# Kernel tuning notes

Measured on AMD Instinct MI355X. Metric: run time of the kernel, lower is better.

Reference implementation:

```python
import jax, jax.numpy as jnp
import numpy as np

B, T, C = 2, 4096, 512
H, DH = 8, 64            # num_heads, num_head_channels (per-head dim after reshape)
COND = 512
SCALE = (DH // H) ** -0.5  # faithful to original: (num_head_channels // num_heads)**-0.5


def setup_inputs() -> dict:
    key = jax.random.key(0)
    ks = jax.random.split(key, 6)
    x = jax.random.normal(ks[0], (B, T, C), dtype=jnp.float32)
    condition = jax.random.normal(ks[1], (B, T, COND), dtype=jnp.float32)
    W_qk = jax.random.normal(ks[2], (COND, 2 * H * DH), dtype=jnp.float32) * (COND ** -0.5)
    W_v = jax.random.normal(ks[3], (C, H * DH), dtype=jnp.float32) * (C ** -0.5)
    W_u = jax.random.normal(ks[4], (H * DH, C), dtype=jnp.float32) * ((H * DH) ** -0.5)
    b_u = jax.random.normal(ks[5], (C,), dtype=jnp.float32) * 0.01
    return {"x": x, "condition": condition, "W_qk": W_qk, "W_v": W_v, "W_u": W_u, "b_u": b_u}


def reference(x, condition, W_qk, W_v, W_u, b_u):
    b, t, _ = x.shape
    qk = condition @ W_qk                                  # [b, t, 2*H*DH]
    q, k = jnp.split(qk, 2, axis=-1)
    q = q.reshape(b, t, H, DH).transpose(0, 2, 1, 3)       # [b, H, t, DH]
    k = k.reshape(b, t, H, DH).transpose(0, 2, 1, 3)
    v = (x @ W_v).reshape(b, t, H, DH).transpose(0, 2, 1, 3)
    q = q * SCALE
    dots = jnp.einsum('bhid,bhjd->bhij', q, k)             # [b, H, t, t] (1 GB score matrix)
    attn = jax.nn.softmax(dots, axis=-1)
    out = jnp.einsum('bhij,bhjd->bhid', attn, v)           # [b, H, t, DH]
    out = out.transpose(0, 2, 1, 3).reshape(b, t, H * DH)
    return out @ W_u + b_u
```

## Files before the change

### kernel.cpp

```cpp
#include <hip/hip_runtime.h>

#define B_SZ 2
#define T_SZ 4096

typedef unsigned short u16;
typedef __attribute__((ext_vector_type(8))) short short8;
typedef __attribute__((ext_vector_type(4))) float f32x4;
typedef __attribute__((ext_vector_type(4))) unsigned short u16x4;

#define CEXP 0.51006973f

__device__ __forceinline__ u16 f2bf(float f) {
    unsigned int u;
    __builtin_memcpy(&u, &f, 4);
    u = (u + 0x7fffu + ((u >> 16) & 1u)) >> 16;
    return (u16)u;
}
__device__ __forceinline__ unsigned int rbits(float f) {
    unsigned int u;
    __builtin_memcpy(&u, &f, 4);
    return u + 0x8000u;
}
__device__ __forceinline__ f32x4 mfma16(short8 a, short8 b, f32x4 c) {
    return __builtin_amdgcn_mfma_f32_16x16x32_bf16(a, b, c, 0, 0, 0);
}

__global__ void k_prep(const float* __restrict__ Wqk, const float* __restrict__ Wv,
                       const float* __restrict__ Wu, u16* __restrict__ Wqk_t,
                       u16* __restrict__ Wv_t, u16* __restrict__ Wu_t) {
    int blk = blockIdx.x, tid = threadIdx.x;
    __shared__ u16 T[64][72];
    const float* src; u16* dst; int N, ti;
    if (blk < 128)      { src = Wqk; dst = Wqk_t; N = 1024; ti = blk; }
    else if (blk < 192) { src = Wv;  dst = Wv_t;  N = 512;  ti = blk - 128; }
    else                { src = Wu;  dst = Wu_t;  N = 512;  ti = blk - 192; }
    int nt = N >> 6;
    int bi = ti / nt, bj = ti - bi * nt;
    int kb = bi * 64, nb = bj * 64;
    int r = tid >> 2, c4 = (tid & 3) * 16;
#pragma unroll
    for (int jj = 0; jj < 4; ++jj) {
        float4 v = *(const float4*)(src + (size_t)(kb + r) * N + nb + c4 + jj * 4);
        u16x4 w = { f2bf(v.x), f2bf(v.y), f2bf(v.z), f2bf(v.w) };
        *(u16x4*)(&T[r][c4 + jj * 4]) = w;
    }
    __syncthreads();
#pragma unroll
    for (int jj = 0; jj < 4; ++jj) {
        int c = c4 + jj * 4;
        u16x4 w = { T[c][r], T[c + 1][r], T[c + 2][r], T[c + 3][r] };
        *(u16x4*)(dst + (size_t)(nb + r) * 512 + kb + c) = w;
    }
}

template <typename OutT, int MODE, bool AF32, bool BF32, int TM, int TN>
__device__ __forceinline__ void gemm_body(int m0, int n0,
                                          const void* __restrict__ Ap, const void* __restrict__ Bp,
                                          const float* __restrict__ bias, OutT* __restrict__ C,
                                          OutT* __restrict__ C2, u16* As, u16* Bs) {
    const int K = 512;
    constexpr int BK = 64;
    constexpr int MI = TM / 32, NJ = TN / 32;
    constexpr int NAF = TM / 16, NAB = TM / 32;
    constexpr int NBF = TN / 16, NBB = TN / 32;
    int tid = threadIdx.x;
    int wave = tid >> 6, lane = tid & 63, l16 = lane & 15, q = lane >> 4;
    int mo = (wave & 1) * (TM / 2), no = (wave >> 1) * (TN / 2);

    f32x4 acc[MI][NJ];
#pragma unroll
    for (int i = 0; i < MI; ++i)
#pragma unroll
        for (int j = 0; j < NJ; ++j) acc[i][j] = (f32x4){0.f, 0.f, 0.f, 0.f};

    const float* Af = (const float*)Ap; const u16* Ab = (const u16*)Ap;
    const float* Bf = (const float*)Bp; const u16* Bb = (const u16*)Bp;

    const float* apf[NAF > 0 ? NAF : 1]; const u16* apb[NAB > 0 ? NAB : 1];
    const float* bpf[NBF > 0 ? NBF : 1]; const u16* bpb[NBB > 0 ? NBB : 1];
    float4 raf[NAF > 0 ? NAF : 1], rbf[NBF > 0 ? NBF : 1];
    short8 rab[NAB > 0 ? NAB : 1], rbb[NBB > 0 ? NBB : 1];

    if constexpr (AF32) {
#pragma unroll
        for (int jj = 0; jj < NAF; ++jj) {
            int id = tid + 256 * jj;
            apf[jj] = Af + (size_t)(m0 + (id >> 4)) * K + (id & 15) * 4;
            raf[jj] = *(const float4*)(apf[jj]);
        }
    } else {
#pragma unroll
        for (int jj = 0; jj < NAB; ++jj) {
            int id = tid + 256 * jj;
            apb[jj] = Ab + (size_t)(m0 + (id >> 3)) * K + (id & 7) * 8;
            rab[jj] = *(const short8*)(apb[jj]);
        }
    }
    if constexpr (BF32) {
#pragma unroll
        for (int jj = 0; jj < NBF; ++jj) {
            int id = tid + 256 * jj;
            bpf[jj] = Bf + (size_t)(n0 + (id >> 4)) * K + (id & 15) * 4;
            rbf[jj] = *(const float4*)(bpf[jj]);
        }
    } else {
#pragma unroll
        for (int jj = 0; jj < NBB; ++jj) {
            int id = tid + 256 * jj;
            bpb[jj] = Bb + (size_t)(n0 + (id >> 3)) * K + (id & 7) * 8;
            rbb[jj] = *(const short8*)(bpb[jj]);
        }
    }

#pragma unroll 1
    for (int k0 = 0; k0 < K; k0 += BK) {
        __syncthreads();
        if constexpr (AF32) {
#pragma unroll
            for (int jj = 0; jj < NAF; ++jj) {
                int id = tid + 256 * jj;
                u16x4 w = { f2bf(raf[jj].x), f2bf(raf[jj].y), f2bf(raf[jj].z), f2bf(raf[jj].w) };
                *(u16x4*)(&As[(id >> 4) * 72 + (id & 15) * 4]) = w;
            }
        } else {
#pragma unroll
            for (int jj = 0; jj < NAB; ++jj) {
                int id = tid + 256 * jj;
                *(short8*)(&As[(id >> 3) * 72 + (id & 7) * 8]) = rab[jj];
            }
        }
        if constexpr (BF32) {
#pragma unroll
            for (int jj = 0; jj < NBF; ++jj) {
                int id = tid + 256 * jj;
                u16x4 w = { f2bf(rbf[jj].x), f2bf(rbf[jj].y), f2bf(rbf[jj].z), f2bf(rbf[jj].w) };
                *(u16x4*)(&Bs[(id >> 4) * 72 + (id & 15) * 4]) = w;
            }
        } else {
#pragma unroll
            for (int jj = 0; jj < NBB; ++jj) {
                int id = tid + 256 * jj;
                *(short8*)(&Bs[(id >> 3) * 72 + (id & 7) * 8]) = rbb[jj];
            }
        }
        __syncthreads();

        int kadv = (k0 + BK < K) ? BK : 0;
        if constexpr (AF32) {
#pragma unroll
            for (int jj = 0; jj < NAF; ++jj) { apf[jj] += kadv; raf[jj] = *(const float4*)(apf[jj]); }
        } else {
#pragma unroll
            for (int jj = 0; jj < NAB; ++jj) { apb[jj] += kadv; rab[jj] = *(const short8*)(apb[jj]); }
        }
        if constexpr (BF32) {
#pragma unroll
            for (int jj = 0; jj < NBF; ++jj) { bpf[jj] += kadv; rbf[jj] = *(const float4*)(bpf[jj]); }
        } else {
#pragma unroll
            for (int jj = 0; jj < NBB; ++jj) { bpb[jj] += kadv; rbb[jj] = *(const short8*)(bpb[jj]); }
        }
        __builtin_amdgcn_sched_barrier(0);

#pragma unroll
        for (int kk = 0; kk < 2; ++kk) {
            short8 af[MI], bf[NJ];
#pragma unroll
            for (int i = 0; i < MI; ++i)
                af[i] = *(const short8*)(&As[(mo + i * 16 + l16) * 72 + kk * 32 + q * 8]);
#pragma unroll
            for (int j = 0; j < NJ; ++j)
                bf[j] = *(const short8*)(&Bs[(no + j * 16 + l16) * 72 + kk * 32 + q * 8]);
#pragma unroll
            for (int i = 0; i < MI; ++i)
#pragma unroll
                for (int j = 0; j < NJ; ++j) acc[i][j] = mfma16(af[i], bf[j], acc[i][j]);
        }
    }

#pragma unroll
    for (int i = 0; i < MI; ++i) {
        int mb = m0 + mo + i * 16 + q * 4;
#pragma unroll
        for (int j = 0; j < NJ; ++j) {
            int nc = n0 + no + j * 16 + l16;
            if constexpr (MODE == 0) {
                float4 bb = *(const float4*)(bias + mb);
                float4 w = { acc[i][j][0] + bb.x, acc[i][j][1] + bb.y,
                             acc[i][j][2] + bb.z, acc[i][j][3] + bb.w };
                *(float4*)(&C[(size_t)nc * 512 + mb]) = w;
            } else if constexpr (MODE == 1) {
                int b = nc >> 12, t = nc & 4095;
                int h = (mb & 511) >> 6, d = mb & 63;
                size_t addr = ((size_t)((b * 8 + h) * 4096 + t)) * 64 + d;
                if (mb < 512) {
                    u16x4 w = { f2bf(acc[i][j][0] * CEXP), f2bf(acc[i][j][1] * CEXP),
                                f2bf(acc[i][j][2] * CEXP), f2bf(acc[i][j][3] * CEXP) };
                    *(u16x4*)(&C[addr]) = w;
                } else {
                    u16x4 w = { f2bf(acc[i][j][0]), f2bf(acc[i][j][1]),
                                f2bf(acc[i][j][2]), f2bf(acc[i][j][3]) };
                    *(u16x4*)(&C2[addr]) = w;
                }
            } else {
                int b = mb >> 12, t = mb & 4095;
                int kt = t >> 6, k64 = t & 63;
                int h = nc >> 6, d = nc & 63;
                size_t addr = ((((size_t)(b * 8 + h) * 64 + kt) * 64 + d) << 6) + k64;
                u16x4 w = { f2bf(acc[i][j][0]), f2bf(acc[i][j][1]),
                            f2bf(acc[i][j][2]), f2bf(acc[i][j][3]) };
                *(u16x4*)(&C[addr]) = w;
            }
        }
    }
}

__global__ __launch_bounds__(256) void k_qkv(const u16* __restrict__ Wqk_t, const float* __restrict__ cond,
                                             const float* __restrict__ x, const u16* __restrict__ Wv_t,
                                             u16* __restrict__ Qh, u16* __restrict__ Kh,
                                             u16* __restrict__ Vb) {
    __shared__ __align__(16) u16 smem[(128 + 128) * 72];
    u16* As = smem;
    u16* Bs = smem + 128 * 72;
    int bid = blockIdx.x;
    if (bid < 512) {
        int bx = bid >> 6, by = bid & 63;
        gemm_body<u16, 1, false, true, 128, 128>(bx * 128, by * 128, Wqk_t, cond, nullptr, Qh, Kh, As, Bs);
    } else {
        int bid2 = bid - 512;
        int by = bid2 >> 6, bx = bid2 & 63;
        gemm_body<u16, 2, true, false, 128, 128>(bx * 128, by * 128, x, Wv_t, nullptr, Vb, nullptr, As, Bs);
    }
}

__global__ __launch_bounds__(256) void k_out(const u16* __restrict__ Wu_t, const u16* __restrict__ at,
                                             const float* __restrict__ bu, float* __restrict__ out) {
    __shared__ __align__(16) u16 smem[(128 + 128) * 72];
    int bid = blockIdx.x;
    int bx = bid >> 6, by = bid & 63;
    gemm_body<float, 0, false, false, 128, 128>(bx * 128, by * 128, Wu_t, at, bu, out, nullptr,
                                                smem, smem + 128 * 72);
}

__global__ __launch_bounds__(512) void k_flash(const u16* __restrict__ Qh, const u16* __restrict__ Kh,
                                               const u16* __restrict__ Vb, u16* __restrict__ o) {
    int bid = blockIdx.x;
    int h = bid & 7, qt = (bid >> 3) & 31, b = bid >> 8;
    int tid = threadIdx.x;
    int wave = tid >> 6, lane = tid & 63, l16 = lane & 15, q = lane >> 4;
    int ks = wave >> 2, w4 = wave & 3;
    int t256 = tid & 255;

    __shared__ __align__(16) u16 smem[19456];
    u16* Kt = smem + ks * 8704;
    u16* Vt = Kt + 64 * 64;

    int head = b * 8 + h;
    short8 qf[2][2];
#pragma unroll
    for (int g = 0; g < 2; ++g) {
        const u16* qp = Qh + ((size_t)head * 4096 + qt * 128 + g * 64 + w4 * 16 + l16) * 64 + q * 8;
        qf[g][0] = *(const short8*)(qp);
        qf[g][1] = *(const short8*)(qp + 32);
    }

    const u16* kb = Kh + (size_t)head * 4096 * 64;
    const u16* vb = Vb + (size_t)head * 4096 * 64;

    int r0 = t256 >> 3, g0 = t256 & 7;
    int sr = (r0 & 3) | (((r0 >> 3) & 1) << 2);
    u16* kw0 = &Kt[r0 * 64 + ((g0 ^ sr) << 3)];
    u16* kw1 = kw0 + 32 * 64;
    u16* vw0 = &Vt[r0 * 72 + g0 * 8];
    u16* vw1 = vw0 + 32 * 72;

    f32x4 oacc[2][4];
#pragma unroll
    for (int g = 0; g < 2; ++g)
#pragma unroll
        for (int c = 0; c < 4; ++c) oacc[g][c] = (f32x4){0.f, 0.f, 0.f, 0.f};
    f32x4 lacc[2];
    lacc[0] = (f32x4){0.f, 0.f, 0.f, 0.f};
    lacc[1] = (f32x4){0.f, 0.f, 0.f, 0.f};
    const short8 ones = { 0x3F80, 0x3F80, 0x3F80, 0x3F80, 0x3F80, 0x3F80, 0x3F80, 0x3F80 };
    int pi0 = (l16 >> 2) * 8 + (l16 & 3);
    int sq = l16 & 7;

    size_t off0 = (size_t)(ks * 32 + (qt & 31)) * 4096;
    short8 rk0 = *(const short8*)(kb + off0 + t256 * 8);
    short8 rk1 = *(const short8*)(kb + off0 + t256 * 8 + 2048);
    short8 rv0 = *(const short8*)(vb + off0 + t256 * 8);
    short8 rv1 = *(const short8*)(vb + off0 + t256 * 8 + 2048);

#pragma unroll 1
    for (int it = 0; it < 32; ++it) {
        __syncthreads();
        *(short8*)kw0 = rk0;
        *(short8*)kw1 = rk1;
        *(short8*)vw0 = rv0;
        *(short8*)vw1 = rv1;
        __syncthreads();

        size_t offn = (size_t)(ks * 32 + ((qt + it + 1) & 31)) * 4096;
        rk0 = *(const short8*)(kb + offn + t256 * 8);
        rk1 = *(const short8*)(kb + offn + t256 * 8 + 2048);
        rv0 = *(const short8*)(vb + offn + t256 * 8);
        rv1 = *(const short8*)(vb + offn + t256 * 8 + 2048);
        __builtin_amdgcn_sched_barrier(0);

        __builtin_amdgcn_s_setprio(1);
#pragma unroll
        for (int kk = 0; kk < 2; ++kk) {
            const u16* ka = &Kt[(kk * 32 + pi0) * 64];
            short8 A00 = *(const short8*)(ka + ((q ^ sq) << 3));
            short8 A01 = *(const short8*)(ka + (((4 | q) ^ sq) << 3));
            short8 A10 = *(const short8*)(ka + 4 * 64 + ((q ^ sq) << 3));
            short8 A11 = *(const short8*)(ka + 4 * 64 + (((4 | q) ^ sq) << 3));
            short8 vfc[4];
#pragma unroll
            for (int c = 0; c < 4; ++c)
                vfc[c] = *(const short8*)(&Vt[(c * 16 + l16) * 72 + kk * 32 + q * 8]);

#pragma unroll
            for (int g = 0; g < 2; ++g) {
                f32x4 s0 = (f32x4){0.f, 0.f, 0.f, 0.f};
                f32x4 s1 = (f32x4){0.f, 0.f, 0.f, 0.f};
                s0 = mfma16(A00, qf[g][0], s0); s0 = mfma16(A01, qf[g][1], s0);
                s1 = mfma16(A10, qf[g][0], s1); s1 = mfma16(A11, qf[g][1], s1);

                uint4 pd;
                pd.x = __builtin_amdgcn_perm(rbits(__builtin_amdgcn_exp2f(s0[1])),
                                             rbits(__builtin_amdgcn_exp2f(s0[0])), 0x07060302u);
                pd.y = __builtin_amdgcn_perm(rbits(__builtin_amdgcn_exp2f(s0[3])),
                                             rbits(__builtin_amdgcn_exp2f(s0[2])), 0x07060302u);
                pd.z = __builtin_amdgcn_perm(rbits(__builtin_amdgcn_exp2f(s1[1])),
                                             rbits(__builtin_amdgcn_exp2f(s1[0])), 0x07060302u);
                pd.w = __builtin_amdgcn_perm(rbits(__builtin_amdgcn_exp2f(s1[3])),
                                             rbits(__builtin_amdgcn_exp2f(s1[2])), 0x07060302u);
                short8 pf;
                __builtin_memcpy(&pf, &pd, 16);

                lacc[g] = mfma16(ones, pf, lacc[g]);
#pragma unroll
                for (int c = 0; c < 4; ++c)
                    oacc[g][c] = mfma16(vfc[c], pf, oacc[g][c]);
            }
        }
        __builtin_amdgcn_s_setprio(0);
    }

    __syncthreads();
    float* red = (float*)smem;
    if (ks == 1) {
        float* rp = red + ((w4 * 64 + lane) * 37);
#pragma unroll
        for (int g = 0; g < 2; ++g)
#pragma unroll
            for (int c = 0; c < 4; ++c)
#pragma unroll
                for (int r = 0; r < 4; ++r) rp[g * 16 + c * 4 + r] = oacc[g][c][r];
        rp[32] = lacc[0][0];
        rp[33] = lacc[1][0];
    }
    __syncthreads();
    if (ks == 0) {
        const float* rp = red + ((w4 * 64 + lane) * 37);
#pragma unroll
        for (int g = 0; g < 2; ++g) {
#pragma unroll
            for (int c = 0; c < 4; ++c)
#pragma unroll
                for (int r = 0; r < 4; ++r) oacc[g][c][r] += rp[g * 16 + c * 4 + r];
            float inv = 1.f / (lacc[g][0] + rp[32 + g]);
            u16* ob = o + (size_t)(b * T_SZ + qt * 128 + g * 64 + w4 * 16 + l16) * 512 + h * 64 + q * 4;
#pragma unroll
            for (int c = 0; c < 4; ++c) {
                u16x4 w = { f2bf(oacc[g][c][0] * inv), f2bf(oacc[g][c][1] * inv),
                            f2bf(oacc[g][c][2] * inv), f2bf(oacc[g][c][3] * inv) };
                *(u16x4*)(ob + c * 16) = w;
            }
        }
    }
}

extern "C" void kernel_launch(void* const* d_in, const int* in_sizes, int n_in,
                              void* d_out, int out_size, void* d_ws, size_t ws_size,
                              hipStream_t stream) {
    const float* x    = (const float*)d_in[0];
    const float* cond = (const float*)d_in[1];
    const float* Wqk  = (const float*)d_in[2];
    const float* Wv   = (const float*)d_in[3];
    const float* Wu   = (const float*)d_in[4];
    const float* bu   = (const float*)d_in[5];
    float* out = (float*)d_out;

    const size_t MT = (size_t)B_SZ * T_SZ;
    u16* qh_ws = (u16*)d_ws;
    u16* kh_ws = qh_ws + MT * 512;
    u16* vb_ws = kh_ws + MT * 512;
    u16* at_ws = vb_ws + MT * 512;
    u16* Wqk_t = at_ws + MT * 512;
    u16* Wv_t  = Wqk_t + (size_t)1024 * 512;
    u16* Wu_t  = Wv_t + (size_t)512 * 512;

    k_prep<<<256, 256, 0, stream>>>(Wqk, Wv, Wu, Wqk_t, Wv_t, Wu_t);
    k_qkv<<<768, 256, 0, stream>>>(Wqk_t, cond, x, Wv_t, qh_ws, kh_ws, vb_ws);
    k_flash<<<512, 512, 0, stream>>>(qh_ws, kh_ws, vb_ws, at_ws);
    k_out<<<256, 256, 0, stream>>>(Wu_t, at_ws, bu, out);
}
```

Before: 207.7 us.

## Fuse all four stages into one persistent kernel with grid barriers

Replaces the four separate launches (weight prep, QKV GEMM, flash attention, output GEMM) with a single 512-block kernel that runs each stage in turn, separated by atomic-counter grid barriers. The GEMMs now use 512-thread blocks with 128x256 tiles, and the register prefetch of the next K slice is dropped, so loads for a slice are issued right before it is used. This removes launch gaps and inter-kernel tail effects. In exchange, many blocks sit idle in the GEMM stages, all blocks must spin at each barrier, and the design depends on all 512 blocks being co-resident to avoid deadlock.

```diff
diff --git a/kernel.cpp b/kernel.cpp
--- a/kernel.cpp
+++ b/kernel.cpp
@@ -25,164 +25,129 @@
     return __builtin_amdgcn_mfma_f32_16x16x32_bf16(a, b, c, 0, 0, 0);
 }
 
-__global__ void k_prep(const float* __restrict__ Wqk, const float* __restrict__ Wv,
-                       const float* __restrict__ Wu, u16* __restrict__ Wqk_t,
-                       u16* __restrict__ Wv_t, u16* __restrict__ Wu_t) {
-    int blk = blockIdx.x, tid = threadIdx.x;
-    __shared__ u16 T[64][72];
-    const float* src; u16* dst; int N, ti;
-    if (blk < 128)      { src = Wqk; dst = Wqk_t; N = 1024; ti = blk; }
-    else if (blk < 192) { src = Wv;  dst = Wv_t;  N = 512;  ti = blk - 128; }
-    else                { src = Wu;  dst = Wu_t;  N = 512;  ti = blk - 192; }
-    int nt = N >> 6;
-    int bi = ti / nt, bj = ti - bi * nt;
-    int kb = bi * 64, nb = bj * 64;
-    int r = tid >> 2, c4 = (tid & 3) * 16;
-#pragma unroll
-    for (int jj = 0; jj < 4; ++jj) {
-        float4 v = *(const float4*)(src + (size_t)(kb + r) * N + nb + c4 + jj * 4);
-        u16x4 w = { f2bf(v.x), f2bf(v.y), f2bf(v.z), f2bf(v.w) };
-        *(u16x4*)(&T[r][c4 + jj * 4]) = w;
-    }
+struct GBar { unsigned int cnt; unsigned int p0[15]; unsigned int gen; unsigned int p1[15]; };
+__device__ GBar g_bar[3];
+#define NBLK 512
+
+__device__ __forceinline__ void gridbar(int i) {
     __syncthreads();
-#pragma unroll
-    for (int jj = 0; jj < 4; ++jj) {
-        int c = c4 + jj * 4;
-        u16x4 w = { T[c][r], T[c + 1][r], T[c + 2][r], T[c + 3][r] };
-        *(u16x4*)(dst + (size_t)(nb + r) * 512 + kb + c) = w;
-    }
-}
-
-template <typename OutT, int MODE, bool AF32, bool BF32, int TM, int TN>
-__device__ __forceinline__ void gemm_body(int m0, int n0,
-                                          const void* __restrict__ Ap, const void* __restrict__ Bp,
-                                          const float* __restrict__ bias, OutT* __restrict__ C,
-                                          OutT* __restrict__ C2, u16* As, u16* Bs) {
+    if (threadIdx.x == 0) {
+        unsigned int g = __hip_atomic_load(&g_bar[i].gen, __ATOMIC_ACQUIRE, __HIP_MEMORY_SCOPE_AGENT);
+        unsigned int a = __hip_atomic_fetch_add(&g_bar[i].cnt, 1u, __ATOMIC_ACQ_REL, __HIP_MEMORY_SCOPE_AGENT);
+        if (a == NBLK - 1u) {
+            __hip_atomic_store(&g_bar[i].cnt, 0u, __ATOMIC_RELAXED, __HIP_MEMORY_SCOPE_AGENT);
+            __hip_atomic_fetch_add(&g_bar[i].gen, 1u, __ATOMIC_RELEASE, __HIP_MEMORY_SCOPE_AGENT);
+        } else {
+            while (__hip_atomic_load(&g_bar[i].gen, __ATOMIC_ACQUIRE, __HIP_MEMORY_SCOPE_AGENT) == g)
+                __builtin_amdgcn_s_sleep(2);
+        }
+    }
+    __syncthreads();
+}
+
+template <typename OutT, int MODE, bool AF32, bool BF32>
+__device__ void gemm512(int m0, int n0, const void* __restrict__ Ap, const void* __restrict__ Bp,
+                        const float* __restrict__ bias, OutT* __restrict__ C,
+                        OutT* __restrict__ C2, u16* smem) {
     const int K = 512;
-    constexpr int BK = 64;
-    constexpr int MI = TM / 32, NJ = TN / 32;
-    constexpr int NAF = TM / 16, NAB = TM / 32;
-    constexpr int NBF = TN / 16, NBB = TN / 32;
+    u16* As = smem;
+    u16* Bs = smem + 128 * 72;
     int tid = threadIdx.x;
     int wave = tid >> 6, lane = tid & 63, l16 = lane & 15, q = lane >> 4;
-    int mo = (wave & 1) * (TM / 2), no = (wave >> 1) * (TN / 2);
-
-    f32x4 acc[MI][NJ];
-#pragma unroll
-    for (int i = 0; i < MI; ++i)
-#pragma unroll
-        for (int j = 0; j < NJ; ++j) acc[i][j] = (f32x4){0.f, 0.f, 0.f, 0.f};
+    int mo = (wave & 1) * 64, no = (wave >> 1) * 64;
+
+    f32x4 acc[4][4];
+#pragma unroll
+    for (int i = 0; i < 4; ++i)
+#pragma unroll
+        for (int j = 0; j < 4; ++j) acc[i][j] = (f32x4){0.f, 0.f, 0.f, 0.f};
 
     const float* Af = (const float*)Ap; const u16* Ab = (const u16*)Ap;
     const float* Bf = (const float*)Bp; const u16* Bb = (const u16*)Bp;
 
-    const float* apf[NAF > 0 ? NAF : 1]; const u16* apb[NAB > 0 ? NAB : 1];
-    const float* bpf[NBF > 0 ? NBF : 1]; const u16* bpb[NBB > 0 ? NBB : 1];
-    float4 raf[NAF > 0 ? NAF : 1], rbf[NBF > 0 ? NBF : 1];
-    short8 rab[NAB > 0 ? NAB : 1], rbb[NBB > 0 ? NBB : 1];
-
-    if constexpr (AF32) {
-#pragma unroll
-        for (int jj = 0; jj < NAF; ++jj) {
-            int id = tid + 256 * jj;
-            apf[jj] = Af + (size_t)(m0 + (id >> 4)) * K + (id & 15) * 4;
-            raf[jj] = *(const float4*)(apf[jj]);
-        }
-    } else {
-#pragma unroll
-        for (int jj = 0; jj < NAB; ++jj) {
-            int id = tid + 256 * jj;
-            apb[jj] = Ab + (size_t)(m0 + (id >> 3)) * K + (id & 7) * 8;
-            rab[jj] = *(const short8*)(apb[jj]);
-        }
-    }
-    if constexpr (BF32) {
-#pragma unroll
-        for (int jj = 0; jj < NBF; ++jj) {
-            int id = tid + 256 * jj;
-            bpf[jj] = Bf + (size_t)(n0 + (id >> 4)) * K + (id & 15) * 4;
-            rbf[jj] = *(const float4*)(bpf[jj]);
-        }
-    } else {
-#pragma unroll
-        for (int jj = 0; jj < NBB; ++jj) {
-            int id = tid + 256 * jj;
-            bpb[jj] = Bb + (size_t)(n0 + (id >> 3)) * K + (id & 7) * 8;
-            rbb[jj] = *(const short8*)(bpb[jj]);
-        }
-    }
-
 #pragma unroll 1
-    for (int k0 = 0; k0 < K; k0 += BK) {
+    for (int k0 = 0; k0 < K; k0 += 64) {
+        float4 raf[AF32 ? 4 : 1]; short8 rab[AF32 ? 1 : 2];
+        float4 rbf[BF32 ? 8 : 1]; short8 rbb[BF32 ? 1 : 4];
+        if constexpr (AF32) {
+#pragma unroll
+            for (int jj = 0; jj < 4; ++jj) {
+                int id = tid + 512 * jj;
+                raf[jj] = *(const float4*)(Af + (size_t)(m0 + (id >> 4)) * K + k0 + (id & 15) * 4);
+            }
+        } else {
+#pragma unroll
+            for (int jj = 0; jj < 2; ++jj) {
+                int id = tid + 512 * jj;
+                rab[jj] = *(const short8*)(Ab + (size_t)(m0 + (id >> 3)) * K + k0 + (id & 7) * 8);
+            }
+        }
+        if constexpr (BF32) {
+#pragma unroll
+            for (int jj = 0; jj < 8; ++jj) {
+                int id = tid + 512 * jj;
+                rbf[jj] = *(const float4*)(Bf + (size_t)(n0 + (id >> 4)) * K + k0 + (id & 15) * 4);
+            }
+        } else {
+#pragma unroll
+            for (int jj = 0; jj < 4; ++jj) {
+                int id = tid + 512 * jj;
+                rbb[jj] = *(const short8*)(Bb + (size_t)(n0 + (id >> 3)) * K + k0 + (id & 7) * 8);
+            }
+        }
+        __builtin_amdgcn_sched_barrier(0);
         __syncthreads();
         if constexpr (AF32) {
 #pragma unroll
-            for (int jj = 0; jj < NAF; ++jj) {
-                int id = tid + 256 * jj;
+            for (int jj = 0; jj < 4; ++jj) {
+                int id = tid + 512 * jj;
                 u16x4 w = { f2bf(raf[jj].x), f2bf(raf[jj].y), f2bf(raf[jj].z), f2bf(raf[jj].w) };
                 *(u16x4*)(&As[(id >> 4) * 72 + (id & 15) * 4]) = w;
             }
         } else {
 #pragma unroll
-            for (int jj = 0; jj < NAB; ++jj) {
-                int id = tid + 256 * jj;
+            for (int jj = 0; jj < 2; ++jj) {
+                int id = tid + 512 * jj;
                 *(short8*)(&As[(id >> 3) * 72 + (id & 7) * 8]) = rab[jj];
             }
         }
         if constexpr (BF32) {
 #pragma unroll
-            for (int jj = 0; jj < NBF; ++jj) {
-                int id = tid + 256 * jj;
+            for (int jj = 0; jj < 8; ++jj) {
+                int id = tid + 512 * jj;
                 u16x4 w = { f2bf(rbf[jj].x), f2bf(rbf[jj].y), f2bf(rbf[jj].z), f2bf(rbf[jj].w) };
                 *(u16x4*)(&Bs[(id >> 4) * 72 + (id & 15) * 4]) = w;
             }
         } else {
 #pragma unroll
-            for (int jj = 0; jj < NBB; ++jj) {
-                int id = tid + 256 * jj;
+            for (int jj = 0; jj < 4; ++jj) {
+                int id = tid + 512 * jj;
                 *(short8*)(&Bs[(id >> 3) * 72 + (id & 7) * 8]) = rbb[jj];
             }
         }
         __syncthreads();
 
-        int kadv = (k0 + BK < K) ? BK : 0;
-        if constexpr (AF32) {
-#pragma unroll
-            for (int jj = 0; jj < NAF; ++jj) { apf[jj] += kadv; raf[jj] = *(const float4*)(apf[jj]); }
-        } else {
-#pragma unroll
-            for (int jj = 0; jj < NAB; ++jj) { apb[jj] += kadv; rab[jj] = *(const short8*)(apb[jj]); }
-        }
-        if constexpr (BF32) {
-#pragma unroll
-            for (int jj = 0; jj < NBF; ++jj) { bpf[jj] += kadv; rbf[jj] = *(const float4*)(bpf[jj]); }
-        } else {
-#pragma unroll
-            for (int jj = 0; jj < NBB; ++jj) { bpb[jj] += kadv; rbb[jj] = *(const short8*)(bpb[jj]); }
-        }
-        __builtin_amdgcn_sched_barrier(0);
-
 #pragma unroll
         for (int kk = 0; kk < 2; ++kk) {
-            short8 af[MI], bf[NJ];
-#pragma unroll
-            for (int i = 0; i < MI; ++i)
+            short8 af[4], bf[4];
+#pragma unroll
+            for (int i = 0; i < 4; ++i)
                 af[i] = *(const short8*)(&As[(mo + i * 16 + l16) * 72 + kk * 32 + q * 8]);
 #pragma unroll
-            for (int j = 0; j < NJ; ++j)
+            for (int j = 0; j < 4; ++j)
                 bf[j] = *(const short8*)(&Bs[(no + j * 16 + l16) * 72 + kk * 32 + q * 8]);
 #pragma unroll
-            for (int i = 0; i < MI; ++i)
-#pragma unroll
-                for (int j = 0; j < NJ; ++j) acc[i][j] = mfma16(af[i], bf[j], acc[i][j]);
-        }
-    }
-
-#pragma unroll
-    for (int i = 0; i < MI; ++i) {
+            for (int i = 0; i < 4; ++i)
+#pragma unroll
+                for (int j = 0; j < 4; ++j) acc[i][j] = mfma16(af[i], bf[j], acc[i][j]);
+        }
+    }
+
+#pragma unroll
+    for (int i = 0; i < 4; ++i) {
         int mb = m0 + mo + i * 16 + q * 4;
 #pragma unroll
-        for (int j = 0; j < NJ; ++j) {
+        for (int j = 0; j < 4; ++j) {
             int nc = n0 + no + j * 16 + l16;
             if constexpr (MODE == 0) {
                 float4 bb = *(const float4*)(bias + mb);
@@ -215,44 +180,15 @@
     }
 }
 
-__global__ __launch_bounds__(256) void k_qkv(const u16* __restrict__ Wqk_t, const float* __restrict__ cond,
-                                             const float* __restrict__ x, const u16* __restrict__ Wv_t,
-                                             u16* __restrict__ Qh, u16* __restrict__ Kh,
-                                             u16* __restrict__ Vb) {
-    __shared__ __align__(16) u16 smem[(128 + 128) * 72];
-    u16* As = smem;
-    u16* Bs = smem + 128 * 72;
-    int bid = blockIdx.x;
-    if (bid < 512) {
-        int bx = bid >> 6, by = bid & 63;
-        gemm_body<u16, 1, false, true, 128, 128>(bx * 128, by * 128, Wqk_t, cond, nullptr, Qh, Kh, As, Bs);
-    } else {
-        int bid2 = bid - 512;
-        int by = bid2 >> 6, bx = bid2 & 63;
-        gemm_body<u16, 2, true, false, 128, 128>(bx * 128, by * 128, x, Wv_t, nullptr, Vb, nullptr, As, Bs);
-    }
-}
-
-__global__ __launch_bounds__(256) void k_out(const u16* __restrict__ Wu_t, const u16* __restrict__ at,
-                                             const float* __restrict__ bu, float* __restrict__ out) {
-    __shared__ __align__(16) u16 smem[(128 + 128) * 72];
-    int bid = blockIdx.x;
-    int bx = bid >> 6, by = bid & 63;
-    gemm_body<float, 0, false, false, 128, 128>(bx * 128, by * 128, Wu_t, at, bu, out, nullptr,
-                                                smem, smem + 128 * 72);
-}
-
-__global__ __launch_bounds__(512) void k_flash(const u16* __restrict__ Qh, const u16* __restrict__ Kh,
-                                               const u16* __restrict__ Vb, u16* __restrict__ o) {
-    int bid = blockIdx.x;
+__device__ void flash_dev(int bid, const u16* __restrict__ Qh, const u16* __restrict__ Kh,
+                          const u16* __restrict__ Vb, u16* __restrict__ o, u16* sm) {
     int h = bid & 7, qt = (bid >> 3) & 31, b = bid >> 8;
     int tid = threadIdx.x;
     int wave = tid >> 6, lane = tid & 63, l16 = lane & 15, q = lane >> 4;
     int ks = wave >> 2, w4 = wave & 3;
     int t256 = tid & 255;
 
-    __shared__ __align__(16) u16 smem[19456];
-    u16* Kt = smem + ks * 8704;
+    u16* Kt = sm + ks * 8704;
     u16* Vt = Kt + 64 * 64;
 
     int head = b * 8 + h;
@@ -350,7 +286,7 @@
     }
 
     __syncthreads();
-    float* red = (float*)smem;
+    float* red = (float*)sm;
     if (ks == 1) {
         float* rp = red + ((w4 * 64 + lane) * 37);
 #pragma unroll
@@ -380,6 +316,62 @@
                 *(u16x4*)(ob + c * 16) = w;
             }
         }
+    }
+}
+
+__global__ __launch_bounds__(512, 4) void k_fused(
+    const float* __restrict__ x, const float* __restrict__ cond,
+    const float* __restrict__ Wqk, const float* __restrict__ Wv,
+    const float* __restrict__ Wu, const float* __restrict__ bu, float* __restrict__ out,
+    u16* __restrict__ Qh, u16* __restrict__ Kh, u16* __restrict__ Vb, u16* __restrict__ at,
+    u16* __restrict__ Wqk_t, u16* __restrict__ Wv_t, u16* __restrict__ Wu_t) {
+    __shared__ __align__(16) u16 smem[27648];
+    int bid = blockIdx.x, tid = threadIdx.x;
+
+    if (bid < 128) {
+        int half = tid >> 8, t256 = tid & 255;
+        int ti = bid * 2 + half;
+        u16 (*T)[72] = (u16(*)[72])(smem + half * 4608);
+        const float* src; u16* dst; int N, tt;
+        if (ti < 128)      { src = Wqk; dst = Wqk_t; N = 1024; tt = ti; }
+        else if (ti < 192) { src = Wv;  dst = Wv_t;  N = 512;  tt = ti - 128; }
+        else               { src = Wu;  dst = Wu_t;  N = 512;  tt = ti - 192; }
+        int nt = N >> 6;
+        int bi = tt / nt, bj = tt - bi * nt;
+        int kb = bi * 64, nb = bj * 64;
+        int r = t256 >> 2, c4 = (t256 & 3) * 16;
+#pragma unroll
+        for (int jj = 0; jj < 4; ++jj) {
+            float4 v = *(const float4*)(src + (size_t)(kb + r) * N + nb + c4 + jj * 4);
+            u16x4 w = { f2bf(v.x), f2bf(v.y), f2bf(v.z), f2bf(v.w) };
+            *(u16x4*)(&T[r][c4 + jj * 4]) = w;
+        }
+        __syncthreads();
+#pragma unroll
+        for (int jj = 0; jj < 4; ++jj) {
+            int c = c4 + jj * 4;
+            u16x4 w = { T[c][r], T[c + 1][r], T[c + 2][r], T[c + 3][r] };
+            *(u16x4*)(dst + (size_t)(nb + r) * 512 + kb + c) = w;
+        }
+    }
+    gridbar(0);
+
+    if (bid < 256) {
+        int bx = bid >> 5, by = bid & 31;
+        gemm512<u16, 1, false, true>(bx * 128, by * 256, Wqk_t, cond, nullptr, Qh, Kh, smem);
+    } else if (bid < 384) {
+        int id2 = bid - 256;
+        int m = id2 & 63, n = id2 >> 6;
+        gemm512<u16, 2, true, false>(m * 128, n * 256, x, Wv_t, nullptr, Vb, nullptr, smem);
+    }
+    gridbar(1);
+
+    flash_dev(bid, Qh, Kh, Vb, at, smem);
+    gridbar(2);
+
+    if (bid < 128) {
+        int bx = bid >> 5, by = bid & 31;
+        gemm512<float, 0, false, false>(bx * 128, by * 256, Wu_t, at, bu, out, nullptr, smem);
     }
 }
 
@@ -403,8 +395,6 @@
     u16* Wv_t  = Wqk_t + (size_t)1024 * 512;
     u16* Wu_t  = Wv_t + (size_t)512 * 512;
 
-    k_prep<<<256, 256, 0, stream>>>(Wqk, Wv, Wu, Wqk_t, Wv_t, Wu_t);
-    k_qkv<<<768, 256, 0, stream>>>(Wqk_t, cond, x, Wv_t, qh_ws, kh_ws, vb_ws);
-    k_flash<<<512, 512, 0, stream>>>(qh_ws, kh_ws, vb_ws, at_ws);
-    k_out<<<256, 256, 0, stream>>>(Wu_t, at_ws, bu, out);
-}
+    k_fused<<<512, 512, 0, stream>>>(x, cond, Wqk, Wv, Wu, bu, out,
+                                     qh_ws, kh_ws, vb_ws, at_ws, Wqk_t, Wv_t, Wu_t);
+}
```

Result: slower. 539.3 us (+159.6%).

## Double the flash-attention KV tile per iteration and swizzle the V LDS layout

Applied to the files above, without the earlier changes.

Each K/V-split group now stages 128 keys per iteration instead of 64, halving the loop trip count and the number of block-wide barriers. V is stored with an XOR swizzle in two 64-wide halves instead of padded rows. Register prefetch doubles to four short8 loads each for K and V per thread, and LDS use grows to 64 KB. This raises register pressure and may lower occupancy.

```diff
diff --git a/kernel.cpp b/kernel.cpp
--- a/kernel.cpp
+++ b/kernel.cpp
@@ -251,9 +251,9 @@
     int ks = wave >> 2, w4 = wave & 3;
     int t256 = tid & 255;
 
-    __shared__ __align__(16) u16 smem[19456];
-    u16* Kt = smem + ks * 8704;
-    u16* Vt = Kt + 64 * 64;
+    __shared__ __align__(16) u16 smem[32768];
+    u16* Kt = smem + ks * 16384;
+    u16* Vt = Kt + 8192;
 
     int head = b * 8 + h;
     short8 qf[2][2];
@@ -269,10 +269,12 @@
 
     int r0 = t256 >> 3, g0 = t256 & 7;
     int sr = (r0 & 3) | (((r0 >> 3) & 1) << 2);
-    u16* kw0 = &Kt[r0 * 64 + ((g0 ^ sr) << 3)];
-    u16* kw1 = kw0 + 32 * 64;
-    u16* vw0 = &Vt[r0 * 72 + g0 * 8];
-    u16* vw1 = vw0 + 32 * 72;
+    u16* kw[4]; u16* vw[4];
+#pragma unroll
+    for (int j = 0; j < 4; ++j) {
+        kw[j] = &Kt[(r0 + 32 * j) * 64 + ((g0 ^ sr) << 3)];
+        vw[j] = &Vt[(j >> 1) * 4096 + (r0 + 32 * (j & 1)) * 64 + ((g0 ^ sr) << 3)];
+    }
 
     f32x4 oacc[2][4];
 #pragma unroll
@@ -285,41 +287,46 @@
     const short8 ones = { 0x3F80, 0x3F80, 0x3F80, 0x3F80, 0x3F80, 0x3F80, 0x3F80, 0x3F80 };
     int pi0 = (l16 >> 2) * 8 + (l16 & 3);
     int sq = l16 & 7;
-
-    size_t off0 = (size_t)(ks * 32 + (qt & 31)) * 4096;
-    short8 rk0 = *(const short8*)(kb + off0 + t256 * 8);
-    short8 rk1 = *(const short8*)(kb + off0 + t256 * 8 + 2048);
-    short8 rv0 = *(const short8*)(vb + off0 + t256 * 8);
-    short8 rv1 = *(const short8*)(vb + off0 + t256 * 8 + 2048);
+    int sv = (l16 & 3) | (((l16 >> 3) & 1) << 2);
+    int st = qt & 15;
+
+    short8 rk[4], rv[4];
+    size_t off0 = (size_t)(ks * 16 + st) * 8192;
+#pragma unroll
+    for (int j = 0; j < 4; ++j) {
+        rk[j] = *(const short8*)(kb + off0 + j * 2048 + t256 * 8);
+        rv[j] = *(const short8*)(vb + off0 + j * 2048 + t256 * 8);
+    }
 
 #pragma unroll 1
-    for (int it = 0; it < 32; ++it) {
+    for (int it = 0; it < 16; ++it) {
         __syncthreads();
-        *(short8*)kw0 = rk0;
-        *(short8*)kw1 = rk1;
-        *(short8*)vw0 = rv0;
-        *(short8*)vw1 = rv1;
+#pragma unroll
+        for (int j = 0; j < 4; ++j) { *(short8*)kw[j] = rk[j]; *(short8*)vw[j] = rv[j]; }
         __syncthreads();
 
-        size_t offn = (size_t)(ks * 32 + ((qt + it + 1) & 31)) * 4096;
-        rk0 = *(const short8*)(kb + offn + t256 * 8);
-        rk1 = *(const short8*)(kb + offn + t256 * 8 + 2048);
-        rv0 = *(const short8*)(vb + offn + t256 * 8);
-        rv1 = *(const short8*)(vb + offn + t256 * 8 + 2048);
+        size_t offn = (size_t)(ks * 16 + ((st + it + 1) & 15)) * 8192;
+#pragma unroll
+        for (int j = 0; j < 4; ++j) {
+            rk[j] = *(const short8*)(kb + offn + j * 2048 + t256 * 8);
+            rv[j] = *(const short8*)(vb + offn + j * 2048 + t256 * 8);
+        }
         __builtin_amdgcn_sched_barrier(0);
 
         __builtin_amdgcn_s_setprio(1);
 #pragma unroll
-        for (int kk = 0; kk < 2; ++kk) {
+        for (int kk = 0; kk < 4; ++kk) {
             const u16* ka = &Kt[(kk * 32 + pi0) * 64];
             short8 A00 = *(const short8*)(ka + ((q ^ sq) << 3));
             short8 A01 = *(const short8*)(ka + (((4 | q) ^ sq) << 3));
             short8 A10 = *(const short8*)(ka + 4 * 64 + ((q ^ sq) << 3));
             short8 A11 = *(const short8*)(ka + 4 * 64 + (((4 | q) ^ sq) << 3));
+            const u16* va = &Vt[(kk >> 1) * 4096];
+            int vg = (((kk & 1) * 4 + q) ^ sv) << 3;
             short8 vfc[4];
 #pragma unroll
             for (int c = 0; c < 4; ++c)
-                vfc[c] = *(const short8*)(&Vt[(c * 16 + l16) * 72 + kk * 32 + q * 8]);
+                vfc[c] = *(const short8*)(va + (c * 16 + l16) * 64 + vg);
 
 #pragma unroll
             for (int g = 0; g < 2; ++g) {
```

Measured after the change: 204.7 us. No clear change (-1.4%).

## Drop KV-split in flash kernel; single 4-wave group iterates all KV tiles

Applied to the files above, without the earlier changes.

The flash attention kernel no longer splits the key/value range across two 4-wave groups with a shared-memory reduction at the end. Instead each 256-thread block walks all 64 KV tiles itself. The V tile moves from a padded layout to an XOR-swizzled 64-wide layout, and the waves alternate the order of the two K sub-chunks to spread out LDS bank access. This removes the final reduction and cuts LDS footprint, which may raise occupancy, but halves the per-block parallelism and doubles the serial loop length.

```diff
diff --git a/kernel.cpp b/kernel.cpp
--- a/kernel.cpp
+++ b/kernel.cpp
@@ -242,18 +242,18 @@
                                                 smem, smem + 128 * 72);
 }
 
-__global__ __launch_bounds__(512) void k_flash(const u16* __restrict__ Qh, const u16* __restrict__ Kh,
+__global__ __launch_bounds__(256) void k_flash(const u16* __restrict__ Qh, const u16* __restrict__ Kh,
                                                const u16* __restrict__ Vb, u16* __restrict__ o) {
     int bid = blockIdx.x;
     int h = bid & 7, qt = (bid >> 3) & 31, b = bid >> 8;
     int tid = threadIdx.x;
     int wave = tid >> 6, lane = tid & 63, l16 = lane & 15, q = lane >> 4;
-    int ks = wave >> 2, w4 = wave & 3;
-    int t256 = tid & 255;
-
-    __shared__ __align__(16) u16 smem[19456];
-    u16* Kt = smem + ks * 8704;
-    u16* Vt = Kt + 64 * 64;
+    int w4 = wave;
+    int t256 = tid;
+
+    __shared__ __align__(16) u16 smem[8192];
+    u16* Kt = smem;
+    u16* Vt = smem + 4096;
 
     int head = b * 8 + h;
     short8 qf[2][2];
@@ -271,8 +271,8 @@
     int sr = (r0 & 3) | (((r0 >> 3) & 1) << 2);
     u16* kw0 = &Kt[r0 * 64 + ((g0 ^ sr) << 3)];
     u16* kw1 = kw0 + 32 * 64;
-    u16* vw0 = &Vt[r0 * 72 + g0 * 8];
-    u16* vw1 = vw0 + 32 * 72;
+    u16* vw0 = &Vt[r0 * 64 + ((g0 ^ sr) << 3)];
+    u16* vw1 = vw0 + 32 * 64;
 
     f32x4 oacc[2][4];
 #pragma unroll
@@ -285,15 +285,19 @@
     const short8 ones = { 0x3F80, 0x3F80, 0x3F80, 0x3F80, 0x3F80, 0x3F80, 0x3F80, 0x3F80 };
     int pi0 = (l16 >> 2) * 8 + (l16 & 3);
     int sq = l16 & 7;
-
-    size_t off0 = (size_t)(ks * 32 + (qt & 31)) * 4096;
-    short8 rk0 = *(const short8*)(kb + off0 + t256 * 8);
-    short8 rk1 = *(const short8*)(kb + off0 + t256 * 8 + 2048);
-    short8 rv0 = *(const short8*)(vb + off0 + t256 * 8);
-    short8 rv1 = *(const short8*)(vb + off0 + t256 * 8 + 2048);
+    int sv = (l16 & 3) | (((l16 >> 3) & 1) << 2);
+    int st = (qt << 1) & 63;
+    int kko = wave & 1;
+
+    short8 rk0, rk1, rv0, rv1;
+    size_t off0 = (size_t)st * 4096;
+    rk0 = *(const short8*)(kb + off0 + t256 * 8);
+    rk1 = *(const short8*)(kb + off0 + t256 * 8 + 2048);
+    rv0 = *(const short8*)(vb + off0 + t256 * 8);
+    rv1 = *(const short8*)(vb + off0 + t256 * 8 + 2048);
 
 #pragma unroll 1
-    for (int it = 0; it < 32; ++it) {
+    for (int it = 0; it < 64; ++it) {
         __syncthreads();
         *(short8*)kw0 = rk0;
         *(short8*)kw1 = rk1;
@@ -301,7 +305,7 @@
         *(short8*)vw1 = rv1;
         __syncthreads();
 
-        size_t offn = (size_t)(ks * 32 + ((qt + it + 1) & 31)) * 4096;
+        size_t offn = (size_t)((st + it + 1) & 63) * 4096;
         rk0 = *(const short8*)(kb + offn + t256 * 8);
         rk1 = *(const short8*)(kb + offn + t256 * 8 + 2048);
         rv0 = *(const short8*)(vb + offn + t256 * 8);
@@ -310,16 +314,18 @@
 
         __builtin_amdgcn_s_setprio(1);
 #pragma unroll
-        for (int kk = 0; kk < 2; ++kk) {
+        for (int kx = 0; kx < 2; ++kx) {
+            int kk = kx ^ kko;
             const u16* ka = &Kt[(kk * 32 + pi0) * 64];
             short8 A00 = *(const short8*)(ka + ((q ^ sq) << 3));
             short8 A01 = *(const short8*)(ka + (((4 | q) ^ sq) << 3));
             short8 A10 = *(const short8*)(ka + 4 * 64 + ((q ^ sq) << 3));
             short8 A11 = *(const short8*)(ka + 4 * 64 + (((4 | q) ^ sq) << 3));
+            int vg = ((kk * 4 + q) ^ sv) << 3;
             short8 vfc[4];
 #pragma unroll
             for (int c = 0; c < 4; ++c)
-                vfc[c] = *(const short8*)(&Vt[(c * 16 + l16) * 72 + kk * 32 + q * 8]);
+                vfc[c] = *(const short8*)(&Vt[(c * 16 + l16) * 64 + vg]);
 
 #pragma unroll
             for (int g = 0; g < 2; ++g) {
@@ -349,36 +355,15 @@
         __builtin_amdgcn_s_setprio(0);
     }
 
-    __syncthreads();
-    float* red = (float*)smem;
-    if (ks == 1) {
-        float* rp = red + ((w4 * 64 + lane) * 37);
-#pragma unroll
-        for (int g = 0; g < 2; ++g)
-#pragma unroll
-            for (int c = 0; c < 4; ++c)
-#pragma unroll
-                for (int r = 0; r < 4; ++r) rp[g * 16 + c * 4 + r] = oacc[g][c][r];
-        rp[32] = lacc[0][0];
-        rp[33] = lacc[1][0];
-    }
-    __syncthreads();
-    if (ks == 0) {
-        const float* rp = red + ((w4 * 64 + lane) * 37);
-#pragma unroll
-        for (int g = 0; g < 2; ++g) {
-#pragma unroll
-            for (int c = 0; c < 4; ++c)
-#pragma unroll
-                for (int r = 0; r < 4; ++r) oacc[g][c][r] += rp[g * 16 + c * 4 + r];
-            float inv = 1.f / (lacc[g][0] + rp[32 + g]);
-            u16* ob = o + (size_t)(b * T_SZ + qt * 128 + g * 64 + w4 * 16 + l16) * 512 + h * 64 + q * 4;
-#pragma unroll
-            for (int c = 0; c < 4; ++c) {
-                u16x4 w = { f2bf(oacc[g][c][0] * inv), f2bf(oacc[g][c][1] * inv),
-                            f2bf(oacc[g][c][2] * inv), f2bf(oacc[g][c][3] * inv) };
-                *(u16x4*)(ob + c * 16) = w;
-            }
+#pragma unroll
+    for (int g = 0; g < 2; ++g) {
+        float inv = 1.f / lacc[g][0];
+        u16* ob = o + (size_t)(b * T_SZ + qt * 128 + g * 64 + w4 * 16 + l16) * 512 + h * 64 + q * 4;
+#pragma unroll
+        for (int c = 0; c < 4; ++c) {
+            u16x4 w = { f2bf(oacc[g][c][0] * inv), f2bf(oacc[g][c][1] * inv),
+                        f2bf(oacc[g][c][2] * inv), f2bf(oacc[g][c][3] * inv) };
+            *(u16x4*)(ob + c * 16) = w;
         }
     }
 }
@@ -405,6 +390,6 @@
 
     k_prep<<<256, 256, 0, stream>>>(Wqk, Wv, Wu, Wqk_t, Wv_t, Wu_t);
     k_qkv<<<768, 256, 0, stream>>>(Wqk_t, cond, x, Wv_t, qh_ws, kh_ws, vb_ws);
-    k_flash<<<512, 512, 0, stream>>>(qh_ws, kh_ws, vb_ws, at_ws);
+    k_flash<<<512, 256, 0, stream>>>(qh_ws, kh_ws, vb_ws, at_ws);
     k_out<<<256, 256, 0, stream>>>(Wu_t, at_ws, bu, out);
 }
```

After: 217.9 us. +4.9%, slower.
